# Performance work log

Hardware: AMD Instinct MI355X
Metric: run time of the kernel (lower is better)

## Reference

```python
import jax, jax.numpy as jnp
import numpy as np


def _squash(s):
    # s: [B, 10, 16]; norms reduce over the capsule-class dim (axis=1), as in torch code
    s_l2 = jnp.linalg.norm(s, axis=1)[:, :, None]   # [B, 16, 1]
    s_l1 = jnp.sum(jnp.abs(s), axis=1)[:, :, None]  # [B, 16, 1]
    return s_l2 / (1.0 + s_l2) * (jnp.swapaxes(s, 1, 2) / s_l1)  # [B, 16, 10]


def setup_inputs() -> dict:
    key = jax.random.key(0)
    ks = jax.random.split(key, 8)
    B = 1024
    x = jax.random.normal(ks[0], (B, 1, 28, 28), dtype=jnp.float32)
    conv1_w = jax.random.normal(ks[1], (256, 1, 9, 9), dtype=jnp.float32) * 0.05
    conv1_b = jnp.zeros((256,), dtype=jnp.float32)
    prim_w = jax.random.normal(ks[2], (32, 32, 1, 9, 9), dtype=jnp.float32) * 0.05
    prim_b = jnp.zeros((32,), dtype=jnp.float32)
    a = float(np.sqrt(6.0 / (8 + 16)))  # xavier-uniform bound for dig_W
    dig_W = jax.random.uniform(ks[3], (1152, 8, 16), jnp.float32, -a, a)
    dig_Wb = jnp.zeros((1152, 16), dtype=jnp.float32)
    out_w = jax.random.normal(ks[4], (10, 10, 16, 1), dtype=jnp.float32) * 0.05
    out_b = jnp.zeros((10,), dtype=jnp.float32)
    return dict(x=x, conv1_w=conv1_w, conv1_b=conv1_b, prim_w=prim_w, prim_b=prim_b,
                dig_W=dig_W, dig_Wb=dig_Wb, out_w=out_w, out_b=out_b)


def reference(x, conv1_w, conv1_b, prim_w, prim_b, dig_W, dig_Wb, out_w, out_b):
    # conv1: [B,1,28,28] -> [B,256,20,20]
    out = jax.lax.conv_general_dilated(
        x, conv1_w, window_strides=(1, 1), padding='VALID',
        dimension_numbers=('NCHW', 'OIHW', 'NCHW')) + conv1_b[None, :, None, None]
    out = jax.nn.relu(out)
    B = out.shape[0]
    out1 = out.reshape(B, 32, 8, 20, 20)
    # prim_layer Conv3d(32,32,[1,9,9],stride=[1,2,2]): -> [B,32,8,6,6]
    out1 = jax.lax.conv_general_dilated(
        out1, prim_w, window_strides=(1, 2, 2), padding='VALID',
        dimension_numbers=('NCDHW', 'OIDHW', 'NCDHW')) + prim_b[None, :, None, None, None]
    out1 = jax.nn.relu(out1)
    out1 = jnp.swapaxes(out1, 2, 4)        # [B,32,6,6,8]
    out1 = out1.reshape(B, 1152, 8)        # primary capsules
    # per-capsule affine: [B,1152,8] x [1152,8,16] -> [B,1152,16]
    u = jnp.einsum('bne,nef->bnf', out1, dig_W) + dig_Wb
    # dynamic routing, 3 iterations
    b = jnp.zeros((B, 10, 1152), dtype=u.dtype)
    v = None
    for _ in range(3):
        c = jax.nn.softmax(b, axis=1)                       # softmax over 10 classes
        s = jnp.einsum('bjn,bnf->bjf', c, u)                # [B,10,16]
        v = _squash(s)                                      # [B,16,10]
        b = b + jnp.swapaxes(jnp.matmul(u, v), 1, 2)        # [B,10,1152]
    # output conv2d(10,10,[16,1]) on [B,10,16,1] == einsum over (class-in, pose)
    logits = jnp.einsum('bif,oif->bo', jnp.swapaxes(v, 1, 2), out_w[..., 0]) + out_b
    return jax.nn.softmax(logits, axis=1)
```

## Files before the change

### kernel.cpp

```cpp
#include <hip/hip_runtime.h>
#include <math.h>

typedef __attribute__((ext_vector_type(8))) short bf16x8;
typedef __attribute__((ext_vector_type(4))) float f32x4;
#define MFMA16(a, b, c) __builtin_amdgcn_mfma_f32_16x16x32_bf16(a, b, c, 0, 0, 0)

union U8 { bf16x8 v; int i4[4]; };
union P4 { unsigned short h[4]; uint2 u2; };

__device__ __forceinline__ unsigned short f2bf(float x) {
    unsigned u = __builtin_bit_cast(unsigned, x);
    unsigned r = (u + 0x7fffu + ((u >> 16) & 1u)) >> 16;
    return (unsigned short)r;
}

__device__ __forceinline__ int koff_of(int kidx) {
    int grp = kidx >> 3, e = kidx & 7;
    if (grp < 9)  return grp * 9 + e;
    if (grp == 9) return e * 9 + 8;
    if (grp == 10) return (e == 0) ? 80 : -1;
    return -1;
}

#define CAPS_BYTES 37748736
#define A1F_ELEMS  24576
#define W3F_ELEMS  82944

__global__ void k_prep(const float* __restrict__ c1w,
                       const float* __restrict__ pw,
                       unsigned short* __restrict__ w1f,
                       unsigned short* __restrict__ w3f)
{
    int idx = blockIdx.x * 256 + threadIdx.x;
    if (idx < A1F_ELEMS) {
        int e = idx & 7, lane = (idx >> 3) & 63, f = idx >> 9;
        int k3 = f % 3, m = (f / 3) & 1, d = f / 6;
        int ch = (lane & 15) + m * 16;
        int kidx = k3 * 32 + ((lane >> 4) << 3) + e;
        int ko = koff_of(kidx);
        w1f[idx] = f2bf(ko >= 0 ? c1w[(ch * 8 + d) * 81 + ko] : 0.f);
    } else if (idx < A1F_ELEMS + W3F_ELEMS) {
        int j = idx - A1F_ELEMS;
        int e = j & 7, lane = (j >> 3) & 63, f = j >> 9;
        int m = f & 1, tap = f >> 1;
        int oc = (lane & 15) + m * 16;
        int i = ((lane >> 4) << 3) + e;
        w3f[j] = f2bf(pw[oc * 2592 + i * 81 + tap]);
    }
}

#define ICS 40

__global__ __launch_bounds__(256, 4) void k_conv(
    const float* __restrict__ x,
    const float* __restrict__ c1b,
    const float* __restrict__ pb,
    const unsigned short* __restrict__ w1f,
    const unsigned short* __restrict__ w3f,
    float* __restrict__ caps)
{
    __shared__ __align__(16) unsigned short img[800];
    __shared__ __align__(16) unsigned short imgs[800];
    __shared__ __align__(16) unsigned short interm[400 * ICS];

    const int t = threadIdx.x;
    const int lane = t & 63, w = t >> 6;
    const int g = lane >> 4, col = lane & 15;
    const int b = blockIdx.x >> 3, d = blockIdx.x & 7;

    for (int idx = t; idx < 784; idx += 256) {
        unsigned short v = f2bf(x[b * 784 + idx]);
        img[idx] = v;
        if (idx > 0) imgs[idx - 1] = v;
    }
    __syncthreads();

    {
        bf16x8 a1[2][3];
        const bf16x8* w1p = (const bf16x8*)w1f;
#pragma unroll
        for (int m = 0; m < 2; ++m)
#pragma unroll
            for (int k3 = 0; k3 < 3; ++k3)
                a1[m][k3] = w1p[((d * 2 + m) * 3 + k3) * 64 + lane];

        float bias[2][4];
#pragma unroll
        for (int m = 0; m < 2; ++m)
#pragma unroll
            for (int r = 0; r < 4; ++r)
                bias[m][r] = c1b[(m * 16 + g * 4 + r) * 8 + d];

        for (int q = w; q < 25; q += 4) {
            int p = q * 16 + col;
            int py = p / 20, px = p - py * 20;
            int base = py * 28 + px;
            const unsigned short* rbase = (base & 1) ? &imgs[base - 1] : &img[base];

            bf16x8 bfrag[3];
#pragma unroll
            for (int k3 = 0; k3 < 2; ++k3) {
                int grp = k3 * 4 + g;
                U8 u8;
#pragma unroll
                for (int qq = 0; qq < 4; ++qq)
                    u8.i4[qq] = *(const int*)(rbase + grp * 28 + 2 * qq);
                bfrag[k3] = u8.v;
            }
            {
                U8 u8;
                if (g == 0) {
#pragma unroll
                    for (int qq = 0; qq < 4; ++qq)
                        u8.i4[qq] = *(const int*)(rbase + 8 * 28 + 2 * qq);
                } else if (g == 1) {
#pragma unroll
                    for (int e = 0; e < 8; ++e)
                        u8.v[e] = (short)img[base + e * 28 + 8];
                } else if (g == 2) {
                    u8.i4[0] = u8.i4[1] = u8.i4[2] = u8.i4[3] = 0;
                    u8.v[0] = (short)img[base + 8 * 28 + 8];
                } else {
                    u8.i4[0] = u8.i4[1] = u8.i4[2] = u8.i4[3] = 0;
                }
                bfrag[2] = u8.v;
            }

            f32x4 acc0 = {0.f, 0.f, 0.f, 0.f};
            f32x4 acc1 = {0.f, 0.f, 0.f, 0.f};
#pragma unroll
            for (int k3 = 0; k3 < 3; ++k3) {
                acc0 = MFMA16(a1[0][k3], bfrag[k3], acc0);
                acc1 = MFMA16(a1[1][k3], bfrag[k3], acc1);
            }
            P4 pk0, pk1;
#pragma unroll
            for (int r = 0; r < 4; ++r) {
                pk0.h[r] = f2bf(fmaxf(acc0[r] + bias[0][r], 0.f));
                pk1.h[r] = f2bf(fmaxf(acc1[r] + bias[1][r], 0.f));
            }
            *(uint2*)(&interm[p * ICS + g * 4])      = pk0.u2;
            *(uint2*)(&interm[p * ICS + 16 + g * 4]) = pk1.u2;
        }
    }
    __syncthreads();

    f32x4 acc[2][3];
#pragma unroll
    for (int m = 0; m < 2; ++m)
#pragma unroll
        for (int nt = 0; nt < 3; ++nt)
            acc[m][nt] = (f32x4){0.f, 0.f, 0.f, 0.f};
    {
        int base2[3];
#pragma unroll
        for (int nt = 0; nt < 3; ++nt) {
            int p2 = nt * 16 + col;
            int xw = p2 / 6, yh = p2 - xw * 6;
            base2[nt] = (p2 < 36) ? (yh * 40 + xw * 2) : 0;
        }
        const bf16x8* w3p = (const bf16x8*)w3f;
        int ky = 0, kx = w;
        for (int tap = w; tap < 81; tap += 4) {
            bf16x8 a0 = w3p[(tap * 2 + 0) * 64 + lane];
            bf16x8 a1v = w3p[(tap * 2 + 1) * 64 + lane];
            int koff = ky * 20 + kx;
#pragma unroll
            for (int nt = 0; nt < 3; ++nt) {
                int pos = base2[nt] + koff;
                bf16x8 bfrag = *(const bf16x8*)(&interm[pos * ICS + g * 8]);
                acc[0][nt] = MFMA16(a0, bfrag, acc[0][nt]);
                acc[1][nt] = MFMA16(a1v, bfrag, acc[1][nt]);
            }
            kx += 4;
            if (kx >= 9) { kx -= 9; ++ky; }
        }
    }
    __syncthreads();
    f32x4* rp = (f32x4*)&interm[0];
    {
#pragma unroll
        for (int m = 0; m < 2; ++m)
#pragma unroll
            for (int nt = 0; nt < 3; ++nt)
                rp[(w * 6 + m * 3 + nt) * 64 + lane] = acc[m][nt];
    }
    __syncthreads();
    for (int idx = t; idx < 384; idx += 256) {
        int tile = idx >> 6, ls = idx & 63;
        f32x4 s = rp[tile * 64 + ls];
#pragma unroll
        for (int ww = 1; ww < 4; ++ww)
            s += rp[(ww * 6 + tile) * 64 + ls];
        int m = tile / 3, nt = tile - m * 3;
        int p2 = nt * 16 + (ls & 15);
        if (p2 < 36) {
            int gr = ls >> 4;
#pragma unroll
            for (int r = 0; r < 4; ++r) {
                int oc = m * 16 + gr * 4 + r;
                caps[(b * 8 + d) * 1152 + oc * 36 + p2] = fmaxf(s[r] + pb[oc], 0.f);
            }
        }
    }
}

#define UST 1156
#define CST 1164

__global__ __launch_bounds__(576) void k_route(
    const float* __restrict__ caps,
    const float* __restrict__ W,
    const float* __restrict__ Wb,
    const float* __restrict__ ow,
    const float* __restrict__ ob,
    float* __restrict__ out)
{
    __shared__ __align__(16) float u[16 * UST];
    __shared__ __align__(16) float c[10 * CST];
    __shared__ __align__(16) float sred[14 * 160];
    __shared__ __align__(16) float vv[16 * 12];
    __shared__ float ss[160];
    __shared__ float red2[16];

    const int t = threadIdx.x;
    const int b = blockIdx.x;
    const int n0 = 2 * t;

    {
        const int nl = t >> 2, fq = t & 3;
        for (int base = 0; base < 1152; base += 144) {
            int n = base + nl;
            float cv[8];
#pragma unroll
            for (int e = 0; e < 8; ++e) cv[e] = caps[(b * 8 + e) * 1152 + n];
            float4 a4 = ((const float4*)(Wb + n * 16))[fq];
#pragma unroll
            for (int e = 0; e < 8; ++e) {
                float4 w4 = ((const float4*)(W + n * 128 + e * 16))[fq];
                a4.x += cv[e] * w4.x; a4.y += cv[e] * w4.y;
                a4.z += cv[e] * w4.z; a4.w += cv[e] * w4.w;
            }
            u[(fq * 4 + 0) * UST + n] = a4.x;
            u[(fq * 4 + 1) * UST + n] = a4.y;
            u[(fq * 4 + 2) * UST + n] = a4.z;
            u[(fq * 4 + 3) * UST + n] = a4.w;
        }
    }
    float breg[2][10];
#pragma unroll
    for (int s = 0; s < 2; ++s)
#pragma unroll
        for (int jj = 0; jj < 10; ++jj) breg[s][jj] = 0.f;
    __syncthreads();

    const int chunk = t / 40, tile = t - chunk * 40;
    const int jp = tile >> 3, fp = tile & 7;
    const bool cact = (chunk < 14);
    const int nbase = chunk * 84;
    const int quads = (chunk == 13) ? 15 : 21;

    for (int iter = 0; iter < 3; ++iter) {
        {
            float cv2[2][10];
#pragma unroll
            for (int s = 0; s < 2; ++s) {
                float m = breg[s][0];
#pragma unroll
                for (int jj = 1; jj < 10; ++jj) m = fmaxf(m, breg[s][jj]);
                float sum = 0.f;
#pragma unroll
                for (int jj = 0; jj < 10; ++jj) { cv2[s][jj] = __expf(breg[s][jj] - m); sum += cv2[s][jj]; }
                float inv = 1.f / sum;
#pragma unroll
                for (int jj = 0; jj < 10; ++jj) cv2[s][jj] *= inv;
            }
#pragma unroll
            for (int jj = 0; jj < 10; ++jj)
                *(float2*)(&c[jj * CST + n0]) = make_float2(cv2[0][jj], cv2[1][jj]);
        }
        __syncthreads();
        if (cact) {
            const f32x4* c0 = (const f32x4*)(c + (2 * jp) * CST + nbase);
            const f32x4* c1 = (const f32x4*)(c + (2 * jp + 1) * CST + nbase);
            const f32x4* u0 = (const f32x4*)(u + (2 * fp) * UST + nbase);
            const f32x4* u1 = (const f32x4*)(u + (2 * fp + 1) * UST + nbase);
            f32x4 a00 = {0,0,0,0}, a01 = {0,0,0,0}, a10 = {0,0,0,0}, a11 = {0,0,0,0};
            for (int q = 0; q < quads; ++q) {
                f32x4 x0 = c0[q], x1 = c1[q], y0 = u0[q], y1 = u1[q];
                a00 += x0 * y0; a01 += x0 * y1;
                a10 += x1 * y0; a11 += x1 * y1;
            }
            f32x4 pk;
            pk.x = a00.x + a00.y + a00.z + a00.w;
            pk.y = a01.x + a01.y + a01.z + a01.w;
            pk.z = a10.x + a10.y + a10.z + a10.w;
            pk.w = a11.x + a11.y + a11.z + a11.w;
            *(f32x4*)(&sred[t * 4]) = pk;
        }
        __syncthreads();
        if (t < 160) {
            int j = t >> 4, f = t & 15;
            int idx0 = ((j >> 1) * 8 + (f >> 1)) * 4 + (j & 1) * 2 + (f & 1);
            float s = 0.f;
#pragma unroll
            for (int ch = 0; ch < 14; ++ch) s += sred[ch * 160 + idx0];
            ss[j * 16 + f] = s;
        }
        __syncthreads();
        if (t < 16) {
            float sv[10], l2 = 0.f, l1 = 0.f;
#pragma unroll
            for (int jj = 0; jj < 10; ++jj) {
                sv[jj] = ss[jj * 16 + t];
                l2 += sv[jj] * sv[jj]; l1 += fabsf(sv[jj]);
            }
            l2 = sqrtf(l2);
            float scale = l2 / (1.f + l2) / l1;
#pragma unroll
            for (int jj = 0; jj < 10; ++jj) vv[t * 12 + jj] = sv[jj] * scale;
        }
        __syncthreads();
        if (iter < 2) {
#pragma unroll
            for (int f = 0; f < 16; ++f) {
                float2 uf = *(const float2*)(&u[f * UST + n0]);
                f32x4 v0 = *(const f32x4*)(&vv[f * 12]);
                f32x4 v1 = *(const f32x4*)(&vv[f * 12 + 4]);
                float2 v2 = *(const float2*)(&vv[f * 12 + 8]);
                breg[0][0] += uf.x * v0.x; breg[1][0] += uf.y * v0.x;
                breg[0][1] += uf.x * v0.y; breg[1][1] += uf.y * v0.y;
                breg[0][2] += uf.x * v0.z; breg[1][2] += uf.y * v0.z;
                breg[0][3] += uf.x * v0.w; breg[1][3] += uf.y * v0.w;
                breg[0][4] += uf.x * v1.x; breg[1][4] += uf.y * v1.x;
                breg[0][5] += uf.x * v1.y; breg[1][5] += uf.y * v1.y;
                breg[0][6] += uf.x * v1.z; breg[1][6] += uf.y * v1.z;
                breg[0][7] += uf.x * v1.w; breg[1][7] += uf.y * v1.w;
                breg[0][8] += uf.x * v2.x; breg[1][8] += uf.y * v2.x;
                breg[0][9] += uf.x * v2.y; breg[1][9] += uf.y * v2.y;
            }
        }
        __syncthreads();
    }

    if (t < 10) {
        float l = ob[t];
#pragma unroll
        for (int i2 = 0; i2 < 10; ++i2)
#pragma unroll
            for (int ff = 0; ff < 16; ++ff)
                l += vv[ff * 12 + i2] * ow[t * 160 + i2 * 16 + ff];
        red2[t] = l;
    }
    __syncthreads();
    if (t == 0) {
        float m = -1e30f;
        for (int o = 0; o < 10; ++o) m = fmaxf(m, red2[o]);
        float sum = 0.f; float e[10];
        for (int o = 0; o < 10; ++o) { e[o] = __expf(red2[o] - m); sum += e[o]; }
        float inv = 1.f / sum;
        for (int o = 0; o < 10; ++o) out[b * 10 + o] = e[o] * inv;
    }
}

extern "C" void kernel_launch(void* const* d_in, const int* in_sizes, int n_in,
                              void* d_out, int out_size, void* d_ws, size_t ws_size,
                              hipStream_t stream) {
    const float* x     = (const float*)d_in[0];
    const float* c1w   = (const float*)d_in[1];
    const float* c1b   = (const float*)d_in[2];
    const float* pw    = (const float*)d_in[3];
    const float* pb    = (const float*)d_in[4];
    const float* digW  = (const float*)d_in[5];
    const float* digWb = (const float*)d_in[6];
    const float* outw  = (const float*)d_in[7];
    const float* outb  = (const float*)d_in[8];
    float* out = (float*)d_out;

    float* caps = (float*)d_ws;
    unsigned short* w1f = (unsigned short*)((char*)d_ws + CAPS_BYTES);
    unsigned short* w3f = w1f + A1F_ELEMS;

    k_prep<<<dim3(420), dim3(256), 0, stream>>>(c1w, pw, w1f, w3f);
    k_conv<<<dim3(8192), dim3(256), 0, stream>>>(x, c1b, pb, w1f, w3f, caps);
    k_route<<<dim3(1024), dim3(576), 0, stream>>>(caps, digW, digWb, outw, outb, out);
}
```

Baseline: 201.9 us.

## Swizzle conv LDS intermediate and move routing s-reduction onto bf16 MFMA

The conv kernel's intermediate LDS buffer now uses an XOR swizzle on byte addresses, replacing the padded-stride layout, to reduce bank conflicts on the bf16x8 fragment reads. The routing kernel stores u and the coupling coefficients c in LDS as bf16 and computes s = c·u with 16x16x32 bf16 MFMA across 9 waves instead of scalar fp32 dot products. Halving the routing LDS footprint and adding a launch-bounds occupancy hint aims at more resident blocks. The cost is reduced precision in u, c and the b-update, which feeds three routing iterations and could change outputs.

```diff
diff --git a/kernel.cpp b/kernel.cpp
--- a/kernel.cpp
+++ b/kernel.cpp
@@ -25,6 +25,8 @@
 #define CAPS_BYTES 37748736
 #define A1F_ELEMS  24576
 #define W3F_ELEMS  82944
+
+#define SWZ(A) ((A) ^ ((((A) >> 7) & 7) << 4))
 
 __global__ void k_prep(const float* __restrict__ c1w,
                        const float* __restrict__ pw,
@@ -61,7 +63,7 @@
 {
     __shared__ __align__(16) unsigned short img[800];
     __shared__ __align__(16) unsigned short imgs[800];
-    __shared__ __align__(16) unsigned short interm[400 * ICS];
+    __shared__ __align__(128) unsigned short interm[400 * ICS];
 
     const int t = threadIdx.x;
     const int lane = t & 63, w = t >> 6;
@@ -139,8 +141,10 @@
                 pk0.h[r] = f2bf(fmaxf(acc0[r] + bias[0][r], 0.f));
                 pk1.h[r] = f2bf(fmaxf(acc1[r] + bias[1][r], 0.f));
             }
-            *(uint2*)(&interm[p * ICS + g * 4])      = pk0.u2;
-            *(uint2*)(&interm[p * ICS + 16 + g * 4]) = pk1.u2;
+            int A0 = p * 80 + g * 8;
+            int A1 = A0 + 32;
+            *(uint2*)((char*)interm + SWZ(A0)) = pk0.u2;
+            *(uint2*)((char*)interm + SWZ(A1)) = pk1.u2;
         }
     }
     __syncthreads();
@@ -152,23 +156,24 @@
         for (int nt = 0; nt < 3; ++nt)
             acc[m][nt] = (f32x4){0.f, 0.f, 0.f, 0.f};
     {
-        int base2[3];
+        int abase[3];
 #pragma unroll
         for (int nt = 0; nt < 3; ++nt) {
             int p2 = nt * 16 + col;
             int xw = p2 / 6, yh = p2 - xw * 6;
-            base2[nt] = (p2 < 36) ? (yh * 40 + xw * 2) : 0;
+            int pos0 = (p2 < 36) ? (yh * 40 + xw * 2) : 0;
+            abase[nt] = pos0 * 80 + g * 16;
         }
         const bf16x8* w3p = (const bf16x8*)w3f;
         int ky = 0, kx = w;
         for (int tap = w; tap < 81; tap += 4) {
             bf16x8 a0 = w3p[(tap * 2 + 0) * 64 + lane];
             bf16x8 a1v = w3p[(tap * 2 + 1) * 64 + lane];
-            int koff = ky * 20 + kx;
+            int koff80 = (ky * 20 + kx) * 80;
 #pragma unroll
             for (int nt = 0; nt < 3; ++nt) {
-                int pos = base2[nt] + koff;
-                bf16x8 bfrag = *(const bf16x8*)(&interm[pos * ICS + g * 8]);
+                int A = abase[nt] + koff80;
+                bf16x8 bfrag = *(const bf16x8*)((const char*)interm + SWZ(A));
                 acc[0][nt] = MFMA16(a0, bfrag, acc[0][nt]);
                 acc[1][nt] = MFMA16(a1v, bfrag, acc[1][nt]);
             }
@@ -205,10 +210,10 @@
     }
 }
 
-#define UST 1156
-#define CST 1164
-
-__global__ __launch_bounds__(576) void k_route(
+#define USB 1160
+#define CSB 1160
+
+__global__ __launch_bounds__(576, 5) void k_route(
     const float* __restrict__ caps,
     const float* __restrict__ W,
     const float* __restrict__ Wb,
@@ -216,14 +221,16 @@
     const float* __restrict__ ob,
     float* __restrict__ out)
 {
-    __shared__ __align__(16) float u[16 * UST];
-    __shared__ __align__(16) float c[10 * CST];
-    __shared__ __align__(16) float sred[14 * 160];
+    __shared__ __align__(16) unsigned short u_bf[16 * USB];
+    __shared__ __align__(16) unsigned short c_bf[10 * CSB];
+    __shared__ __align__(16) float sred[9 * 256];
     __shared__ __align__(16) float vv[16 * 12];
     __shared__ float ss[160];
     __shared__ float red2[16];
 
     const int t = threadIdx.x;
+    const int lane = t & 63, wv = t >> 6;
+    const int g = lane >> 4, col = lane & 15;
     const int b = blockIdx.x;
     const int n0 = 2 * t;
 
@@ -241,10 +248,10 @@
                 a4.x += cv[e] * w4.x; a4.y += cv[e] * w4.y;
                 a4.z += cv[e] * w4.z; a4.w += cv[e] * w4.w;
             }
-            u[(fq * 4 + 0) * UST + n] = a4.x;
-            u[(fq * 4 + 1) * UST + n] = a4.y;
-            u[(fq * 4 + 2) * UST + n] = a4.z;
-            u[(fq * 4 + 3) * UST + n] = a4.w;
+            u_bf[(fq * 4 + 0) * USB + n] = f2bf(a4.x);
+            u_bf[(fq * 4 + 1) * USB + n] = f2bf(a4.y);
+            u_bf[(fq * 4 + 2) * USB + n] = f2bf(a4.z);
+            u_bf[(fq * 4 + 3) * USB + n] = f2bf(a4.w);
         }
     }
     float breg[2][10];
@@ -254,11 +261,7 @@
         for (int jj = 0; jj < 10; ++jj) breg[s][jj] = 0.f;
     __syncthreads();
 
-    const int chunk = t / 40, tile = t - chunk * 40;
-    const int jp = tile >> 3, fp = tile & 7;
-    const bool cact = (chunk < 14);
-    const int nbase = chunk * 84;
-    const int quads = (chunk == 13) ? 15 : 21;
+    const int jrow = (col < 10) ? col : 9;
 
     for (int iter = 0; iter < 3; ++iter) {
         {
@@ -276,35 +279,30 @@
                 for (int jj = 0; jj < 10; ++jj) cv2[s][jj] *= inv;
             }
 #pragma unroll
-            for (int jj = 0; jj < 10; ++jj)
-                *(float2*)(&c[jj * CST + n0]) = make_float2(cv2[0][jj], cv2[1][jj]);
-        }
-        __syncthreads();
-        if (cact) {
-            const f32x4* c0 = (const f32x4*)(c + (2 * jp) * CST + nbase);
-            const f32x4* c1 = (const f32x4*)(c + (2 * jp + 1) * CST + nbase);
-            const f32x4* u0 = (const f32x4*)(u + (2 * fp) * UST + nbase);
-            const f32x4* u1 = (const f32x4*)(u + (2 * fp + 1) * UST + nbase);
-            f32x4 a00 = {0,0,0,0}, a01 = {0,0,0,0}, a10 = {0,0,0,0}, a11 = {0,0,0,0};
-            for (int q = 0; q < quads; ++q) {
-                f32x4 x0 = c0[q], x1 = c1[q], y0 = u0[q], y1 = u1[q];
-                a00 += x0 * y0; a01 += x0 * y1;
-                a10 += x1 * y0; a11 += x1 * y1;
-            }
-            f32x4 pk;
-            pk.x = a00.x + a00.y + a00.z + a00.w;
-            pk.y = a01.x + a01.y + a01.z + a01.w;
-            pk.z = a10.x + a10.y + a10.z + a10.w;
-            pk.w = a11.x + a11.y + a11.z + a11.w;
-            *(f32x4*)(&sred[t * 4]) = pk;
+            for (int jj = 0; jj < 10; ++jj) {
+                unsigned pk = (unsigned)f2bf(cv2[0][jj]) | ((unsigned)f2bf(cv2[1][jj]) << 16);
+                *(unsigned*)(&c_bf[jj * CSB + n0]) = pk;
+            }
+        }
+        __syncthreads();
+        {
+            f32x4 sp = {0.f, 0.f, 0.f, 0.f};
+#pragma unroll
+            for (int mf = 0; mf < 4; ++mf) {
+                int nk = wv * 128 + mf * 32 + g * 8;
+                bf16x8 af = *(const bf16x8*)(&c_bf[jrow * CSB + nk]);
+                bf16x8 bf = *(const bf16x8*)(&u_bf[col * USB + nk]);
+                sp = MFMA16(af, bf, sp);
+            }
+            *(f32x4*)(&sred[wv * 256 + lane * 4]) = sp;
         }
         __syncthreads();
         if (t < 160) {
             int j = t >> 4, f = t & 15;
-            int idx0 = ((j >> 1) * 8 + (f >> 1)) * 4 + (j & 1) * 2 + (f & 1);
+            int li = ((j >> 2) * 16 + f) * 4 + (j & 3);
             float s = 0.f;
 #pragma unroll
-            for (int ch = 0; ch < 14; ++ch) s += sred[ch * 160 + idx0];
+            for (int ww = 0; ww < 9; ++ww) s += sred[ww * 256 + li];
             ss[j * 16 + f] = s;
         }
         __syncthreads();
@@ -324,20 +322,22 @@
         if (iter < 2) {
 #pragma unroll
             for (int f = 0; f < 16; ++f) {
-                float2 uf = *(const float2*)(&u[f * UST + n0]);
+                unsigned pair = *(const unsigned*)(&u_bf[f * USB + n0]);
+                float ux = __builtin_bit_cast(float, pair << 16);
+                float uy = __builtin_bit_cast(float, pair & 0xffff0000u);
                 f32x4 v0 = *(const f32x4*)(&vv[f * 12]);
                 f32x4 v1 = *(const f32x4*)(&vv[f * 12 + 4]);
                 float2 v2 = *(const float2*)(&vv[f * 12 + 8]);
-                breg[0][0] += uf.x * v0.x; breg[1][0] += uf.y * v0.x;
-                breg[0][1] += uf.x * v0.y; breg[1][1] += uf.y * v0.y;
-                breg[0][2] += uf.x * v0.z; breg[1][2] += uf.y * v0.z;
-                breg[0][3] += uf.x * v0.w; breg[1][3] += uf.y * v0.w;
-                breg[0][4] += uf.x * v1.x; breg[1][4] += uf.y * v1.x;
-                breg[0][5] += uf.x * v1.y; breg[1][5] += uf.y * v1.y;
-                breg[0][6] += uf.x * v1.z; breg[1][6] += uf.y * v1.z;
-                breg[0][7] += uf.x * v1.w; breg[1][7] += uf.y * v1.w;
-                breg[0][8] += uf.x * v2.x; breg[1][8] += uf.y * v2.x;
-                breg[0][9] += uf.x * v2.y; breg[1][9] += uf.y * v2.y;
+                breg[0][0] += ux * v0.x; breg[1][0] += uy * v0.x;
+                breg[0][1] += ux * v0.y; breg[1][1] += uy * v0.y;
+                breg[0][2] += ux * v0.z; breg[1][2] += uy * v0.z;
+                breg[0][3] += ux * v0.w; breg[1][3] += uy * v0.w;
+                breg[0][4] += ux * v1.x; breg[1][4] += uy * v1.x;
+                breg[0][5] += ux * v1.y; breg[1][5] += uy * v1.y;
+                breg[0][6] += ux * v1.z; breg[1][6] += uy * v1.z;
+                breg[0][7] += ux * v1.w; breg[1][7] += uy * v1.w;
+                breg[0][8] += ux * v2.x; breg[1][8] += uy * v2.x;
+                breg[0][9] += ux * v2.y; breg[1][9] += uy * v2.y;
             }
         }
         __syncthreads();
```

Result: faster. 187.7 us (-7.1%).
